# Kernel optimization log

Measured on AMD Instinct MI355X. Metric: run time of the kernel, lower is better.

The kernel has to match this reference:

```python
import jax, jax.numpy as jnp
import numpy as np

N_NODES = 100000
N_EDGES = 1600000
D_IN = 128
D_OUT = 128


def setup_inputs() -> dict:
    key = jax.random.key(0)
    k = jax.random.split(key, 7)
    x = jax.random.normal(k[0], (N_NODES, D_IN), dtype=jnp.float32)
    edge_index = jax.random.randint(k[1], (2, N_EDGES), 0, N_NODES, dtype=jnp.int32)
    # MLP params (PyTorch Linear-style scaling)
    s1 = 1.0 / np.sqrt(D_IN)
    s2 = 1.0 / np.sqrt(D_OUT)
    W1 = jax.random.uniform(k[2], (D_IN, D_OUT), jnp.float32, -s1, s1)
    b1 = jax.random.uniform(k[3], (D_OUT,), jnp.float32, -s1, s1)
    W2 = jax.random.uniform(k[4], (D_OUT, D_OUT), jnp.float32, -s2, s2)
    b2 = jax.random.uniform(k[5], (D_OUT,), jnp.float32, -s2, s2)
    eps = jnp.zeros((), dtype=jnp.float32)  # train_eps=True, init 0
    return {"x": x, "edge_index": edge_index, "W1": W1, "b1": b1, "W2": W2, "b2": b2, "eps": eps}


def reference(x, edge_index, W1, b1, W2, b2, eps):
    src, dst = edge_index[0], edge_index[1]  # flow: source_to_target
    # scatter-add neighbor aggregation: agg[i] = sum_{(j->i)} x[j]
    agg = jax.ops.segment_sum(x[src], dst, num_segments=x.shape[0])  # [N, D_IN]
    h = (1.0 + eps) * x + agg
    # 2-layer MLP: Linear -> ReLU -> Linear
    h = jax.nn.relu(h @ W1 + b1)
    return h @ W2 + b2
```

## Files before the change

### kernel.cpp

```cpp
#include <hip/hip_runtime.h>

#define NN    100000
#define NE    1600000
#define DD    128
#define CAP   64
#define NBKT  391
#define PCAP  4608
#define EPB   4096

typedef float  f4v __attribute__((ext_vector_type(4)));
typedef short  s8v __attribute__((ext_vector_type(8)));
typedef unsigned short u16;
typedef unsigned int   u32;

static __device__ __forceinline__ u16 f2bf(float f) {
    u32 u = __float_as_uint(f);
    return (u16)((u + 0x7fffu + ((u >> 16) & 1u)) >> 16);
}
static __device__ __forceinline__ float blo(u32 p) { return __uint_as_float(p << 16); }
static __device__ __forceinline__ float bhi(u32 p) { return __uint_as_float(p & 0xffff0000u); }

__global__ __launch_bounds__(256) void prep_cvt(
    const float* __restrict__ x,
    const float* __restrict__ W1, const float* __restrict__ W2,
    u32* __restrict__ xbp, u16* __restrict__ img1, u16* __restrict__ img2,
    int* __restrict__ gcnt)
{
    const int b   = blockIdx.x;
    const int tid = threadIdx.x;
    if (b < 25000) {
        const int row  = b * 4 + (tid >> 6);
        const int lane = tid & 63;
        const float* xp = x + (size_t)row * DD;
        xbp[(size_t)row * 64 + lane] =
            (u32)f2bf(xp[lane]) | ((u32)f2bf(xp[lane + 64]) << 16);
    } else if (b < 25008) {
        const int gid  = (b - 25000) * 256 + tid;
        const int frag = gid >> 6;
        const int lane = gid & 63;
        const int n  = (frag >> 2) * 16 + (lane & 15);
        const int k0 = (frag & 3) * 32 + (lane >> 4) * 8;
        u16* o1 = img1 + (size_t)gid * 8;
        u16* o2 = img2 + (size_t)gid * 8;
#pragma unroll
        for (int j = 0; j < 8; ++j) {
            o1[j] = f2bf(W1[(size_t)(k0 + j) * DD + n]);
            o2[j] = f2bf(W2[(size_t)(k0 + j) * DD + n]);
        }
    } else {
        const int i = (b - 25008) * 256 + tid;
        if (i < NBKT * 16) gcnt[i] = 0;
    }
}

__global__ __launch_bounds__(256) void part_kernel(
    const int* __restrict__ ei, u32* __restrict__ pairs, int* __restrict__ gcnt)
{
    __shared__ int hist[NBKT];
    __shared__ int base[NBKT];
    const int tid = threadIdx.x;
    const int e0  = blockIdx.x * EPB;
    const int e1  = min(e0 + EPB, NE);

    for (int i = tid; i < NBKT; i += 256) hist[i] = 0;
    __syncthreads();

    for (int e = e0 + tid; e < e1; e += 256)
        atomicAdd(&hist[ei[NE + e] >> 8], 1);
    __syncthreads();

    for (int i = tid; i < NBKT; i += 256) {
        const int h = hist[i];
        base[i] = h ? atomicAdd(&gcnt[i * 16], h) : 0;
        hist[i] = 0;
    }
    __syncthreads();

    for (int e = e0 + tid; e < e1; e += 256) {
        const int s = ei[e];
        const int d = ei[NE + e];
        const int bk = d >> 8;
        const int r  = base[bk] + atomicAdd(&hist[bk], 1);
        if (r < PCAP)
            pairs[(size_t)bk * PCAP + r] = ((u32)s << 8) | (u32)(d & 255);
    }
}

__global__ __launch_bounds__(256) void build_kernel(
    const u32* __restrict__ pairs, const int* __restrict__ gcnt,
    int* __restrict__ cnt, int* __restrict__ eidx)
{
    __shared__ int cl[256], cur[256];
    const int b   = blockIdx.x;
    const int tid = threadIdx.x;
    const int n   = min(gcnt[b * 16], PCAP);
    const u32* pp = pairs + (size_t)b * PCAP;

    cl[tid] = 0; cur[tid] = 0;
    __syncthreads();

    for (int i = tid; i < n; i += 256)
        atomicAdd(&cl[pp[i] & 255], 1);
    __syncthreads();

    const int g = b * 256 + tid;
    if (g < NN) cnt[g] = cl[tid];

    for (int i = tid; i < n; i += 256) {
        const u32 p  = pp[i];
        const int ld = p & 255;
        const int r  = atomicAdd(&cur[ld], 1);
        if (r < CAP) eidx[(size_t)(b * 256 + ld) * CAP + r] = (int)(p >> 8);
    }
}

__global__ __launch_bounds__(256) void gather_kernel(
    const u32* __restrict__ xbp, const int* __restrict__ cnt,
    const int* __restrict__ eidx, const float* __restrict__ epsp,
    u16* __restrict__ hb)
{
    const int node = blockIdx.x * 4 + (threadIdx.x >> 6);
    const int lane = threadIdx.x & 63;
    const int deg  = min(cnt[node], CAP);
    const int base = node * CAP;

    float a[8] = {};
    float c[8] = {};

    int j = 0;
    for (; j + 8 <= deg; j += 8) {
        int  si[8];
        u32  pi[8];
#pragma unroll
        for (int t = 0; t < 8; ++t) si[t] = eidx[base + j + t];
#pragma unroll
        for (int t = 0; t < 8; ++t) pi[t] = xbp[(size_t)si[t] * 64 + lane];
#pragma unroll
        for (int t = 0; t < 8; ++t) { a[t] += blo(pi[t]); c[t] += bhi(pi[t]); }
    }
    if (j + 4 <= deg) {
        int si[4]; u32 pi[4];
#pragma unroll
        for (int t = 0; t < 4; ++t) si[t] = eidx[base + j + t];
#pragma unroll
        for (int t = 0; t < 4; ++t) pi[t] = xbp[(size_t)si[t] * 64 + lane];
#pragma unroll
        for (int t = 0; t < 4; ++t) { a[t] += blo(pi[t]); c[t] += bhi(pi[t]); }
        j += 4;
    }
    for (; j < deg; ++j) {
        const u32 p = xbp[(size_t)eidx[base + j] * 64 + lane];
        a[0] += blo(p); c[0] += bhi(p);
    }

    const float sc = 1.0f + epsp[0];
    const u32 ps = xbp[(size_t)node * 64 + lane];
    const float r0 = sc * blo(ps) + ((a[0]+a[1]) + (a[2]+a[3])) + ((a[4]+a[5]) + (a[6]+a[7]));
    const float r1 = sc * bhi(ps) + ((c[0]+c[1]) + (c[2]+c[3])) + ((c[4]+c[5]) + (c[6]+c[7]));
    hb[(size_t)node * DD + lane]      = f2bf(r0);
    hb[(size_t)node * DD + lane + 64] = f2bf(r1);
}

__global__ __launch_bounds__(256) void mlp_kernel(
    const u16* __restrict__ hb,
    const u16* __restrict__ img1, const u16* __restrict__ img2,
    const float* __restrict__ b1, const float* __restrict__ b2,
    float* __restrict__ out)
{
    __shared__ char lds_raw[4 * 8448];
    const int tid  = threadIdx.x;
    const int wave = tid >> 6;
    const int lane = tid & 63;
    const int l15  = lane & 15;
    const int quad = lane >> 4;

    float* fstage = (float*)(lds_raw + wave * 8448);
    u16*   hstage = (u16*)fstage;

    int rbase = (blockIdx.x * 4 + wave) * 16;
    if (rbase > NN - 16) rbase = NN - 16;

    float bv1[8], bv2[8];
#pragma unroll
    for (int nt = 0; nt < 8; ++nt) {
        bv1[nt] = b1[nt * 16 + l15];
        bv2[nt] = b2[nt * 16 + l15];
    }

    s8v afrag[4];
#pragma unroll
    for (int kc = 0; kc < 4; ++kc)
        afrag[kc] = *(const s8v*)(hb + (size_t)(rbase + l15) * DD + kc * 32 + quad * 8);

    f4v acc1[8] = {};
#pragma unroll
    for (int kc = 0; kc < 4; ++kc)
#pragma unroll
        for (int nt = 0; nt < 8; ++nt) {
            const s8v bfr = *(const s8v*)(img1 + ((size_t)((nt * 4 + kc) * 64 + lane)) * 8);
            acc1[nt] = __builtin_amdgcn_mfma_f32_16x16x32_bf16(afrag[kc], bfr, acc1[nt], 0, 0, 0);
        }

#pragma unroll
    for (int nt = 0; nt < 8; ++nt)
#pragma unroll
        for (int r = 0; r < 4; ++r) {
            const float v = fmaxf(acc1[nt][r] + bv1[nt], 0.0f);
            hstage[(quad * 4 + r) * 136 + nt * 16 + l15] = f2bf(v);
        }
    __syncthreads();

    s8v a2[4];
#pragma unroll
    for (int kc = 0; kc < 4; ++kc)
        a2[kc] = *(const s8v*)&hstage[l15 * 136 + kc * 32 + quad * 8];

    f4v acc2[8] = {};
#pragma unroll
    for (int kc = 0; kc < 4; ++kc)
#pragma unroll
        for (int nt = 0; nt < 8; ++nt) {
            const s8v bfr = *(const s8v*)(img2 + ((size_t)((nt * 4 + kc) * 64 + lane)) * 8);
            acc2[nt] = __builtin_amdgcn_mfma_f32_16x16x32_bf16(a2[kc], bfr, acc2[nt], 0, 0, 0);
        }

    __syncthreads();
#pragma unroll
    for (int nt = 0; nt < 8; ++nt)
#pragma unroll
        for (int r = 0; r < 4; ++r)
            fstage[(quad * 4 + r) * 132 + nt * 16 + l15] = acc2[nt][r] + bv2[nt];
    __syncthreads();

#pragma unroll
    for (int i = 0; i < 8; ++i) {
        const int m  = (lane >> 5) + 2 * i;
        const int c4 = lane & 31;
        const f4v v = *(const f4v*)&fstage[m * 132 + c4 * 4];
        *(f4v*)(out + (size_t)(rbase + m) * DD + c4 * 4) = v;
    }
}

extern "C" void kernel_launch(void* const* d_in, const int* in_sizes, int n_in,
                              void* d_out, int out_size, void* d_ws, size_t ws_size,
                              hipStream_t stream) {
    const float* x   = (const float*)d_in[0];
    const int*   ei  = (const int*)d_in[1];
    const float* W1  = (const float*)d_in[2];
    const float* b1  = (const float*)d_in[3];
    const float* W2  = (const float*)d_in[4];
    const float* b2  = (const float*)d_in[5];
    const float* eps = (const float*)d_in[6];
    float* out = (float*)d_out;

    u32* xbp   = (u32*)d_ws;
    u16* hb    = (u16*)(xbp + (size_t)NN * 64);
    int* eidx  = (int*)(hb + (size_t)NN * DD);
    int* cnt   = eidx + (size_t)NN * CAP;
    u16* img1  = (u16*)(cnt + NN);
    u16* img2  = img1 + (size_t)DD * DD;
    u32* pairs = (u32*)(img2 + (size_t)DD * DD);
    int* gcnt  = (int*)(pairs + (size_t)NBKT * PCAP);

    prep_cvt     <<<25033,              256, 0, stream>>>(x, W1, W2, xbp, img1, img2, gcnt);
    part_kernel  <<<(NE + EPB - 1)/EPB, 256, 0, stream>>>(ei, pairs, gcnt);
    build_kernel <<<NBKT,               256, 0, stream>>>(pairs, gcnt, cnt, eidx);
    gather_kernel<<<NN / 4,             256, 0, stream>>>(xbp, cnt, eidx, eps, hb);
    mlp_kernel   <<<(NN / 16 + 3) / 4,  256, 0, stream>>>(hb, img1, img2, b1, b2, out);
}
```

Baseline: 255.4 us.

## Preload edges into registers and gather neighbors via wave-wide index readlane

The partition and build kernels now load each thread's edge data into register arrays once, up front, instead of re-reading global memory in each pass. The gather kernel loads a node's 64 neighbor indices with one coalesced wave load and broadcasts them with readlane. Padding lanes point to a zeroed sentinel row, so the gather runs in fixed batches of 16 or 8 without scalar tail loops. The sentinel row and larger unrolled batches add wasted loads for low-degree nodes and raise register pressure.

```diff
diff --git a/kernel.cpp b/kernel.cpp
--- a/kernel.cpp
+++ b/kernel.cpp
@@ -47,9 +47,11 @@
             o1[j] = f2bf(W1[(size_t)(k0 + j) * DD + n]);
             o2[j] = f2bf(W2[(size_t)(k0 + j) * DD + n]);
         }
-    } else {
+    } else if (b < 25033) {
         const int i = (b - 25008) * 256 + tid;
         if (i < NBKT * 16) gcnt[i] = 0;
+    } else {
+        if (tid < 64) xbp[(size_t)NN * 64 + tid] = 0;
     }
 }
 
@@ -60,13 +62,21 @@
     __shared__ int base[NBKT];
     const int tid = threadIdx.x;
     const int e0  = blockIdx.x * EPB;
-    const int e1  = min(e0 + EPB, NE);
+
+    int sv[16], dv[16];
+#pragma unroll
+    for (int t = 0; t < 16; ++t) {
+        const int e = e0 + t * 256 + tid;
+        if (e < NE) { sv[t] = ei[e]; dv[t] = ei[NE + e]; }
+        else        { dv[t] = -1; sv[t] = 0; }
+    }
 
     for (int i = tid; i < NBKT; i += 256) hist[i] = 0;
     __syncthreads();
 
-    for (int e = e0 + tid; e < e1; e += 256)
-        atomicAdd(&hist[ei[NE + e] >> 8], 1);
+#pragma unroll
+    for (int t = 0; t < 16; ++t)
+        if (dv[t] >= 0) atomicAdd(&hist[dv[t] >> 8], 1);
     __syncthreads();
 
     for (int i = tid; i < NBKT; i += 256) {
@@ -76,14 +86,14 @@
     }
     __syncthreads();
 
-    for (int e = e0 + tid; e < e1; e += 256) {
-        const int s = ei[e];
-        const int d = ei[NE + e];
-        const int bk = d >> 8;
-        const int r  = base[bk] + atomicAdd(&hist[bk], 1);
-        if (r < PCAP)
-            pairs[(size_t)bk * PCAP + r] = ((u32)s << 8) | (u32)(d & 255);
-    }
+#pragma unroll
+    for (int t = 0; t < 16; ++t)
+        if (dv[t] >= 0) {
+            const int bk = dv[t] >> 8;
+            const int r  = base[bk] + atomicAdd(&hist[bk], 1);
+            if (r < PCAP)
+                pairs[(size_t)bk * PCAP + r] = ((u32)sv[t] << 8) | (u32)(dv[t] & 255);
+        }
 }
 
 __global__ __launch_bounds__(256) void build_kernel(
@@ -96,21 +106,35 @@
     const int n   = min(gcnt[b * 16], PCAP);
     const u32* pp = pairs + (size_t)b * PCAP;
 
+    u32 pv[18];
+#pragma unroll
+    for (int t = 0; t < 18; ++t) {
+        const int i = t * 256 + tid;
+        if (i < n) pv[t] = pp[i];
+    }
+
     cl[tid] = 0; cur[tid] = 0;
     __syncthreads();
 
-    for (int i = tid; i < n; i += 256)
-        atomicAdd(&cl[pp[i] & 255], 1);
+#pragma unroll
+    for (int t = 0; t < 18; ++t) {
+        const int i = t * 256 + tid;
+        if (i < n) atomicAdd(&cl[pv[t] & 255], 1);
+    }
     __syncthreads();
 
     const int g = b * 256 + tid;
     if (g < NN) cnt[g] = cl[tid];
 
-    for (int i = tid; i < n; i += 256) {
-        const u32 p  = pp[i];
-        const int ld = p & 255;
-        const int r  = atomicAdd(&cur[ld], 1);
-        if (r < CAP) eidx[(size_t)(b * 256 + ld) * CAP + r] = (int)(p >> 8);
+#pragma unroll
+    for (int t = 0; t < 18; ++t) {
+        const int i = t * 256 + tid;
+        if (i < n) {
+            const u32 p  = pv[t];
+            const int ld = p & 255;
+            const int r  = atomicAdd(&cur[ld], 1);
+            if (r < CAP) eidx[(size_t)(b * 256 + ld) * CAP + r] = (int)(p >> 8);
+        }
     }
 }
 
@@ -122,41 +146,47 @@
     const int node = blockIdx.x * 4 + (threadIdx.x >> 6);
     const int lane = threadIdx.x & 63;
     const int deg  = min(cnt[node], CAP);
-    const int base = node * CAP;
-
-    float a[8] = {};
-    float c[8] = {};
+
+    int idxv = eidx[(size_t)node * CAP + lane];
+    if (lane >= deg) idxv = NN;
+
+    float a[4] = {}, c[4] = {};
+
+    auto batch16 = [&](int j) {
+        u32 p[16];
+#pragma unroll
+        for (int t = 0; t < 16; ++t) {
+            const int s = __builtin_amdgcn_readlane(idxv, j + t);
+            const u32* row = xbp + ((size_t)(u32)s << 6);
+            p[t] = row[lane];
+        }
+#pragma unroll
+        for (int t = 0; t < 16; ++t) { a[t & 3] += blo(p[t]); c[t & 3] += bhi(p[t]); }
+    };
+    auto batch8 = [&](int j) {
+        u32 p[8];
+#pragma unroll
+        for (int t = 0; t < 8; ++t) {
+            const int s = __builtin_amdgcn_readlane(idxv, j + t);
+            const u32* row = xbp + ((size_t)(u32)s << 6);
+            p[t] = row[lane];
+        }
+#pragma unroll
+        for (int t = 0; t < 8; ++t) { a[t & 3] += blo(p[t]); c[t & 3] += bhi(p[t]); }
+    };
 
     int j = 0;
-    for (; j + 8 <= deg; j += 8) {
-        int  si[8];
-        u32  pi[8];
-#pragma unroll
-        for (int t = 0; t < 8; ++t) si[t] = eidx[base + j + t];
-#pragma unroll
-        for (int t = 0; t < 8; ++t) pi[t] = xbp[(size_t)si[t] * 64 + lane];
-#pragma unroll
-        for (int t = 0; t < 8; ++t) { a[t] += blo(pi[t]); c[t] += bhi(pi[t]); }
-    }
-    if (j + 4 <= deg) {
-        int si[4]; u32 pi[4];
-#pragma unroll
-        for (int t = 0; t < 4; ++t) si[t] = eidx[base + j + t];
-#pragma unroll
-        for (int t = 0; t < 4; ++t) pi[t] = xbp[(size_t)si[t] * 64 + lane];
-#pragma unroll
-        for (int t = 0; t < 4; ++t) { a[t] += blo(pi[t]); c[t] += bhi(pi[t]); }
-        j += 4;
-    }
-    for (; j < deg; ++j) {
-        const u32 p = xbp[(size_t)eidx[base + j] * 64 + lane];
-        a[0] += blo(p); c[0] += bhi(p);
+    for (; j + 16 <= deg; j += 16) batch16(j);
+    const int rem = deg - j;
+    if (rem > 0) {
+        if (rem <= 8) batch8(j);
+        else          batch16(j);
     }
 
     const float sc = 1.0f + epsp[0];
     const u32 ps = xbp[(size_t)node * 64 + lane];
-    const float r0 = sc * blo(ps) + ((a[0]+a[1]) + (a[2]+a[3])) + ((a[4]+a[5]) + (a[6]+a[7]));
-    const float r1 = sc * bhi(ps) + ((c[0]+c[1]) + (c[2]+c[3])) + ((c[4]+c[5]) + (c[6]+c[7]));
+    const float r0 = sc * blo(ps) + ((a[0] + a[1]) + (a[2] + a[3]));
+    const float r1 = sc * bhi(ps) + ((c[0] + c[1]) + (c[2] + c[3]));
     hb[(size_t)node * DD + lane]      = f2bf(r0);
     hb[(size_t)node * DD + lane + 64] = f2bf(r1);
 }
@@ -254,7 +284,7 @@
     float* out = (float*)d_out;
 
     u32* xbp   = (u32*)d_ws;
-    u16* hb    = (u16*)(xbp + (size_t)NN * 64);
+    u16* hb    = (u16*)(xbp + (size_t)(NN + 1) * 64);
     int* eidx  = (int*)(hb + (size_t)NN * DD);
     int* cnt   = eidx + (size_t)NN * CAP;
     u16* img1  = (u16*)(cnt + NN);
@@ -262,7 +292,7 @@
     u32* pairs = (u32*)(img2 + (size_t)DD * DD);
     int* gcnt  = (int*)(pairs + (size_t)NBKT * PCAP);
 
-    prep_cvt     <<<25033,              256, 0, stream>>>(x, W1, W2, xbp, img1, img2, gcnt);
+    prep_cvt     <<<25034,              256, 0, stream>>>(x, W1, W2, xbp, img1, img2, gcnt);
     part_kernel  <<<(NE + EPB - 1)/EPB, 256, 0, stream>>>(ei, pairs, gcnt);
     build_kernel <<<NBKT,               256, 0, stream>>>(pairs, gcnt, cnt, eidx);
     gather_kernel<<<NN / 4,             256, 0, stream>>>(xbp, cnt, eidx, eps, hb);
```

New measurement: 228.5 us. 1.12x faster.
